# Optimization experiments

Hardware: AMD Instinct MI355X
Metric: run time of the kernel (lower is better)

## Reference

```python
import jax, jax.numpy as jnp
import numpy as np

VOCAB = 50000
D = 128      # word_embedding_size
H = 64       # attention_hidden_dim


def _doc_embed(words, emb_table, w_self, b_self):
    """words: (..., W) int -> (..., D) via tanh self-attention pooling over words."""
    we = emb_table[words]                                # (..., W, D)
    scores = jnp.tanh(we @ w_self + b_self)              # (..., W, 1)
    wgt = jax.nn.softmax(scores, axis=-2)                # softmax over word dim
    return jnp.sum(wgt * we, axis=-2)                    # (..., D)


def _attention(reviews_emb, query_emb, Wq, bq, w_red):
    """reviews_emb: (B,R,D), query_emb: (B,1,D) -> (B,D)."""
    B = query_emb.shape[0]
    pq = jnp.tanh(query_emb.reshape(B, D) @ Wq + bq)     # (B, D*H)
    pq = pq.reshape(B, D, H)
    s = jnp.einsum('brd,bdh->brh', reviews_emb, pq)      # (B,R,H)
    r = s @ w_red                                        # (B,R,1)
    w = jax.nn.softmax(r, axis=1)                        # softmax over reviews
    return jnp.sum(w * reviews_emb, axis=1)              # (B,D)


def setup_inputs() -> dict:
    key = jax.random.key(0)
    ks = jax.random.split(key, 9)
    B, R, W = 256, 20, 100
    user = jax.random.randint(ks[0], (B, R, W), 0, VOCAB)
    item = jax.random.randint(ks[1], (B, R, W), 0, VOCAB)
    query = jax.random.randint(ks[2], (B, W), 0, VOCAB)
    emb_table = jax.random.normal(ks[3], (VOCAB, D), dtype=jnp.float32) * 0.01
    w_self = jax.random.normal(ks[4], (D, 1), dtype=jnp.float32) * (1.0 / np.sqrt(D))
    b_self = jax.random.uniform(ks[5], (1,), dtype=jnp.float32, maxval=0.01)
    Wq = jax.random.normal(ks[6], (D, D * H), dtype=jnp.float32) * (1.0 / np.sqrt(D))
    bq = jax.random.uniform(ks[7], (D * H,), dtype=jnp.float32, maxval=0.01)
    w_red = jax.random.normal(ks[8], (H, 1), dtype=jnp.float32) * (1.0 / np.sqrt(H))
    pf = jnp.float32(0.5)  # personalized_factor
    return {"user_reviews_words": user, "item_reviews_words": item, "query": query,
            "emb_table": emb_table, "w_self": w_self, "b_self": b_self,
            "Wq": Wq, "bq": bq, "w_red": w_red, "pf": pf}


def reference(user_reviews_words, item_reviews_words, query,
              emb_table, w_self, b_self, Wq, bq, w_red, pf):
    # mode == 'test'
    user_emb = _doc_embed(user_reviews_words, emb_table, w_self, b_self)   # (B,R,D)
    item_emb = _doc_embed(item_reviews_words, emb_table, w_self, b_self)   # (B,R,D)
    q_emb = _doc_embed(query[:, None, :], emb_table, w_self, b_self)       # (B,1,D)
    user_entity = _attention(user_emb, q_emb, Wq, bq, w_red)               # (B,D)
    item_entity = _attention(item_emb, q_emb, Wq, bq, w_red)               # (B,D)
    personalized = user_entity + pf * q_emb[:, 0, :]
    return (personalized, item_entity)
```

## Files before the change

### kernel.cpp

```cpp
#include <hip/hip_runtime.h>
#include <math.h>

#define D 128
#define H 64
#define W 100
#define R 20
#define NB 256
#define NDOC_UI (NB * R)
#define VOCAB 50000

__device__ __forceinline__ float fast_tanh(float x) {
    float u = __expf(2.0f * x);
    return 1.0f - 2.0f * __builtin_amdgcn_rcpf(1.0f + u);
}
__device__ __forceinline__ float fast_exp_tanh(float x) {
    return __expf(fast_tanh(x));
}

__device__ __forceinline__ unsigned short f2bf(float f) {
    unsigned int b = __float_as_uint(f);
    b += 0x7fffu + ((b >> 16) & 1u);
    return (unsigned short)(b >> 16);
}

__global__ __launch_bounds__(256) void vocab_prep_kernel(
    const float* __restrict__ emb, const float* __restrict__ w_self,
    const float* __restrict__ b_self,
    ushort* __restrict__ emb_bf, float* __restrict__ evocab)
{
    int tid = threadIdx.x, lane32 = tid & 31, grp = tid >> 5;
    int row = blockIdx.x * 8 + grp;
    float4 v   = ((const float4*)emb)[row * 32 + lane32];
    float4 ws4 = ((const float4*)w_self)[lane32];
    float p = v.x * ws4.x + v.y * ws4.y + v.z * ws4.z + v.w * ws4.w;
    p += __shfl_xor(p, 16, 64);
    p += __shfl_xor(p, 8, 64);
    p += __shfl_xor(p, 4, 64);
    p += __shfl_xor(p, 2, 64);
    p += __shfl_xor(p, 1, 64);
    float e = __expf(tanhf(p + b_self[0]));
    if (lane32 == 0) evocab[row] = e;
    ushort4 u;
    u.x = f2bf(v.x * e); u.y = f2bf(v.y * e);
    u.z = f2bf(v.z * e); u.w = f2bf(v.w * e);
    ((ushort4*)emb_bf)[row * 32 + lane32] = u;
}

__global__ __launch_bounds__(128) void doc_embed_bf16_kernel(
    const int* __restrict__ user_w, const int* __restrict__ item_w,
    const int* __restrict__ query_w,
    const ushort* __restrict__ emb_bf, const float* __restrict__ evocab,
    float* __restrict__ user_emb, float* __restrict__ item_emb,
    float* __restrict__ q_emb)
{
    int tid    = threadIdx.x;
    int lane32 = tid & 31;
    int grp    = tid >> 5;
    int doc    = blockIdx.x * 4 + grp;

    const int* wp; float* outp;
    if (doc < NDOC_UI)        { wp = user_w + doc * W;               outp = user_emb + doc * D; }
    else if (doc < 2*NDOC_UI) { int t = doc - NDOC_UI;   wp = item_w  + t * W; outp = item_emb + t * D; }
    else                      { int t = doc - 2*NDOC_UI; wp = query_w + t * W; outp = q_emb    + t * D; }

    int wreg[4];
    #pragma unroll
    for (int k = 0; k < 4; ++k) {
        int idx = k * 32 + lane32;
        wreg[k] = wp[idx > W - 1 ? W - 1 : idx];
    }

    float ep = 0.f;
    #pragma unroll
    for (int k = 0; k < 4; ++k) {
        float e = evocab[wreg[k]];
        if (k < 3 || lane32 < 4) ep += e;
    }
    ep += __shfl_xor(ep, 16, 64);
    ep += __shfl_xor(ep, 8, 64);
    ep += __shfl_xor(ep, 4, 64);
    ep += __shfl_xor(ep, 2, 64);
    ep += __shfl_xor(ep, 1, 64);
    float inv = 1.f / ep;

    int permbase = (tid & 32) << 2;
    int sub      = lane32 >> 4;
    int quad     = lane32 & 15;

    float acc[8];
    #pragma unroll
    for (int j = 0; j < 8; ++j) acc[j] = 0.f;

    const uint4* ebf4 = (const uint4*)emb_bf;

    #pragma unroll
    for (int c = 0; c < 5; ++c) {
        int wid[10]; uint4 v[10];
        #pragma unroll
        for (int j = 0; j < 10; ++j) {
            int s = c * 10 + j;
            int lane_src = ((2 * s) & 31) | sub;
            wid[j] = __builtin_amdgcn_ds_bpermute(permbase | (lane_src << 2),
                                                  wreg[s >> 4]);
        }
        #pragma unroll
        for (int j = 0; j < 10; ++j)
            v[j] = ebf4[(size_t)(unsigned)wid[j] * 16 + quad];
        #pragma unroll
        for (int j = 0; j < 10; ++j) {
            uint4 x = v[j];
            acc[0] += __uint_as_float(x.x << 16);
            acc[1] += __uint_as_float(x.x & 0xffff0000u);
            acc[2] += __uint_as_float(x.y << 16);
            acc[3] += __uint_as_float(x.y & 0xffff0000u);
            acc[4] += __uint_as_float(x.z << 16);
            acc[5] += __uint_as_float(x.z & 0xffff0000u);
            acc[6] += __uint_as_float(x.w << 16);
            acc[7] += __uint_as_float(x.w & 0xffff0000u);
        }
    }

    #pragma unroll
    for (int j = 0; j < 8; ++j) acc[j] += __shfl_xor(acc[j], 16, 64);

    if (lane32 < 16) {
        float4 o0 = make_float4(acc[0]*inv, acc[1]*inv, acc[2]*inv, acc[3]*inv);
        float4 o1 = make_float4(acc[4]*inv, acc[5]*inv, acc[6]*inv, acc[7]*inv);
        ((float4*)outp)[quad * 2]     = o0;
        ((float4*)outp)[quad * 2 + 1] = o1;
    }
}

__global__ __launch_bounds__(256, 7) void doc_embed_fp32_kernel(
    const int* __restrict__ user_w, const int* __restrict__ item_w,
    const int* __restrict__ query_w,
    const float* __restrict__ emb, const float* __restrict__ w_self,
    const float* __restrict__ b_self,
    float* __restrict__ user_emb, float* __restrict__ item_emb,
    float* __restrict__ q_emb)
{
    int tid    = threadIdx.x;
    int lane32 = tid & 31;
    int grp    = tid >> 5;
    int doc    = blockIdx.x * 8 + grp;

    const int* wp; float* outp;
    if (doc < NDOC_UI)        { wp = user_w + doc * W;               outp = user_emb + doc * D; }
    else if (doc < 2*NDOC_UI) { int t = doc - NDOC_UI;   wp = item_w  + t * W; outp = item_emb + t * D; }
    else                      { int t = doc - 2*NDOC_UI; wp = query_w + t * W; outp = q_emb    + t * D; }

    int wreg[4];
    #pragma unroll
    for (int k = 0; k < 4; ++k) {
        int idx = k * 32 + lane32;
        wreg[k] = wp[idx > W - 1 ? W - 1 : idx];
    }

    float4 ws4 = ((const float4*)w_self)[lane32];
    float  bs  = b_self[0];
    const float4* emb4 = (const float4*)emb;
    int permbase = (tid & 32) * 4;

    float4 acc  = make_float4(0.f, 0.f, 0.f, 0.f);
    float  esum = 0.f;

    #pragma unroll
    for (int c = 0; c < 10; ++c) {
        int word[10];
        #pragma unroll
        for (int j = 0; j < 10; ++j) {
            int w = c * 10 + j;
            word[j] = __builtin_amdgcn_ds_bpermute(permbase | ((w & 31) * 4),
                                                   wreg[w >> 5]);
        }
        float4 v[10];
        #pragma unroll
        for (int j = 0; j < 10; ++j)
            v[j] = emb4[(size_t)word[j] * 32 + lane32];

        #pragma unroll
        for (int j = 0; j < 10; ++j) {
            float p = v[j].x * ws4.x + v[j].y * ws4.y + v[j].z * ws4.z + v[j].w * ws4.w;
            p += __shfl_xor(p, 16, 64);
            p += __shfl_xor(p, 8, 64);
            p += __shfl_xor(p, 4, 64);
            p += __shfl_xor(p, 2, 64);
            p += __shfl_xor(p, 1, 64);
            float e = fast_exp_tanh(p + bs);
            esum += e;
            acc.x += e * v[j].x;
            acc.y += e * v[j].y;
            acc.z += e * v[j].z;
            acc.w += e * v[j].w;
        }
    }

    float inv = 1.0f / esum;
    acc.x *= inv; acc.y *= inv; acc.z *= inv; acc.w *= inv;
    ((float4*)outp)[lane32] = acc;
}

__global__ __launch_bounds__(256) void pv_kernel(
    const float* __restrict__ q_emb, const float* __restrict__ Wq,
    const float* __restrict__ bq, const float* __restrict__ w_red,
    float* __restrict__ pv)
{
    __shared__ __align__(16) float Wb[128 * 68];

    int dd  = blockIdx.x;
    int m0g = blockIdx.y * 128;
    int tid = threadIdx.x;

    {
        int rrow = tid >> 4;
        int f4   = tid & 15;
        #pragma unroll
        for (int pass = 0; pass < 8; ++pass) {
            int k = pass * 16 + rrow;
            float4 vw = ((const float4*)Wq)[k * 2048 + dd * 16 + f4];
            *(float4*)&Wb[k * 68 + f4 * 4] = vw;
        }
    }
    __syncthreads();

    int nthr = tid & 15;
    int mthr = tid >> 4;
    int n0 = nthr * 4;
    const float4* q4 = (const float4*)q_emb;
    int mbase = (m0g + mthr * 8) * 32;

    float acc[8][4];
    #pragma unroll
    for (int i = 0; i < 8; ++i)
        #pragma unroll
        for (int j = 0; j < 4; ++j) acc[i][j] = 0.f;

    float4 qa[8], qb[8];
    #pragma unroll
    for (int i = 0; i < 8; ++i) qa[i] = q4[mbase + i * 32];

    for (int k4 = 0; k4 < 32; ++k4) {
        if (k4 < 31) {
            #pragma unroll
            for (int i = 0; i < 8; ++i) qb[i] = q4[mbase + i * 32 + k4 + 1];
        }
        #pragma unroll
        for (int kk = 0; kk < 4; ++kk) {
            float4 wv = *(const float4*)&Wb[(k4 * 4 + kk) * 68 + n0];
            #pragma unroll
            for (int i = 0; i < 8; ++i) {
                float a = (kk == 0) ? qa[i].x : (kk == 1) ? qa[i].y
                        : (kk == 2) ? qa[i].z : qa[i].w;
                acc[i][0] += a * wv.x;
                acc[i][1] += a * wv.y;
                acc[i][2] += a * wv.z;
                acc[i][3] += a * wv.w;
            }
        }
        #pragma unroll
        for (int i = 0; i < 8; ++i) qa[i] = qb[i];
    }

    float4 bqv = ((const float4*)bq)[dd * 16 + nthr];
    float4 wrv = ((const float4*)w_red)[nthr];

    #pragma unroll
    for (int i = 0; i < 8; ++i) {
        float s = fast_tanh(acc[i][0] + bqv.x) * wrv.x
                + fast_tanh(acc[i][1] + bqv.y) * wrv.y
                + fast_tanh(acc[i][2] + bqv.z) * wrv.z
                + fast_tanh(acc[i][3] + bqv.w) * wrv.w;
        s += __shfl_xor(s, 1, 64);
        s += __shfl_xor(s, 2, 64);
        s += __shfl_xor(s, 4, 64);
        s += __shfl_xor(s, 8, 64);
        if (nthr == 0) pv[(m0g + mthr * 8 + i) * 128 + dd] = s;
    }
}

__global__ __launch_bounds__(256) void attn_kernel(
    const float* __restrict__ user_emb, const float* __restrict__ item_emb,
    const float* __restrict__ q_emb, const float* __restrict__ pv,
    const float* __restrict__ pf, float* __restrict__ out)
{
    __shared__ float rev[R * 129];
    __shared__ float pvl[D];
    __shared__ float sc[R];

    int b   = blockIdx.x;
    int set = blockIdx.y;
    const float* revg = (set == 0 ? user_emb : item_emb) + b * R * D;
    int tid = threadIdx.x;

    for (int idx = tid; idx < R * D; idx += 256)
        rev[(idx >> 7) * 129 + (idx & 127)] = revg[idx];
    if (tid < D) pvl[tid] = pv[b * D + tid];
    __syncthreads();

    if (tid < R) {
        float s = 0.f;
        const float* row = &rev[tid * 129];
        #pragma unroll 16
        for (int k = 0; k < D; ++k) s += row[k] * pvl[k];
        sc[tid] = s;
    }
    __syncthreads();

    float m = -1e30f;
    for (int r = 0; r < R; ++r) m = fmaxf(m, sc[r]);
    float sum = 0.f;
    for (int r = 0; r < R; ++r) sum += __expf(sc[r] - m);
    float inv = 1.f / sum;

    if (tid < D) {
        float acc = 0.f;
        for (int r = 0; r < R; ++r)
            acc += __expf(sc[r] - m) * inv * rev[r * 129 + tid];
        if (set == 0) {
            acc += pf[0] * q_emb[b * D + tid];
            out[b * D + tid] = acc;
        } else {
            out[NB * D + b * D + tid] = acc;
        }
    }
}

extern "C" void kernel_launch(void* const* d_in, const int* in_sizes, int n_in,
                              void* d_out, int out_size, void* d_ws, size_t ws_size,
                              hipStream_t stream) {
    const int*   user_w  = (const int*)d_in[0];
    const int*   item_w  = (const int*)d_in[1];
    const int*   query_w = (const int*)d_in[2];
    const float* emb     = (const float*)d_in[3];
    const float* w_self  = (const float*)d_in[4];
    const float* b_self  = (const float*)d_in[5];
    const float* Wq      = (const float*)d_in[6];
    const float* bq      = (const float*)d_in[7];
    const float* w_red   = (const float*)d_in[8];
    const float* pf      = (const float*)d_in[9];

    float* ws       = (float*)d_ws;
    float* user_emb = ws;
    float* item_emb = user_emb + NDOC_UI * D;
    float* q_emb    = item_emb + NDOC_UI * D;
    float* pv       = q_emb    + NB * D;
    float* evocab   = pv       + NB * D;
    ushort* emb_bf  = (ushort*)(evocab + VOCAB);
    float* out      = (float*)d_out;

    const size_t need_fast =
        (size_t)(2 * NDOC_UI * D + 2 * NB * D + VOCAB) * sizeof(float)
        + (size_t)VOCAB * D * sizeof(ushort);

    if (ws_size >= need_fast) {
        vocab_prep_kernel<<<VOCAB / 8, 256, 0, stream>>>(
            emb, w_self, b_self, emb_bf, evocab);
        doc_embed_bf16_kernel<<<(2 * NDOC_UI + NB) / 4, 128, 0, stream>>>(
            user_w, item_w, query_w, emb_bf, evocab, user_emb, item_emb, q_emb);
    } else {
        doc_embed_fp32_kernel<<<(2 * NDOC_UI + NB) / 8, 256, 0, stream>>>(
            user_w, item_w, query_w, emb, w_self, b_self, user_emb, item_emb, q_emb);
    }
    pv_kernel<<<dim3(128, 2), 256, 0, stream>>>(q_emb, Wq, bq, w_red, pv);
    attn_kernel<<<dim3(NB, 2), 256, 0, stream>>>(user_emb, item_emb, q_emb, pv, pf, out);
}
```

Baseline: 152.7 us.

## Split bf16 embedding table into column halves pinned to XCD groups for L2 locality

The prescaled bf16 embedding table is now stored as two column halves of 64 features each. The doc-embed grid is doubled, and block indices are mapped so that four XCDs process one half and the other four process the other half. Each XCD's L2 then only has to cache about half of the gathered table (around 6.4MB instead of 12.8MB), which should raise hit rates on the random gathers. The cost is that every word index and every evocab normalisation sum is now read and computed twice, and each 32-lane group covers 4 words × 8 lanes with an extra shuffle-reduce step.

```diff
diff --git a/kernel.cpp b/kernel.cpp
--- a/kernel.cpp
+++ b/kernel.cpp
@@ -7,6 +7,7 @@
 #define R 20
 #define NB 256
 #define NDOC_UI (NB * R)
+#define NDOC    (2 * NDOC_UI + NB)
 #define VOCAB 50000
 
 __device__ __forceinline__ float fast_tanh(float x) {
@@ -43,7 +44,9 @@
     ushort4 u;
     u.x = f2bf(v.x * e); u.y = f2bf(v.y * e);
     u.z = f2bf(v.z * e); u.w = f2bf(v.w * e);
-    ((ushort4*)emb_bf)[row * 32 + lane32] = u;
+    int half = lane32 >> 4;
+    ushort4* dst = (ushort4*)(emb_bf + (size_t)half * VOCAB * 64);
+    dst[row * 16 + (lane32 & 15)] = u;
 }
 
 __global__ __launch_bounds__(128) void doc_embed_bf16_kernel(
@@ -56,7 +59,11 @@
     int tid    = threadIdx.x;
     int lane32 = tid & 31;
     int grp    = tid >> 5;
-    int doc    = blockIdx.x * 4 + grp;
+    unsigned B   = blockIdx.x;
+    unsigned xcd = B & 7;
+    unsigned half= xcd >> 2;
+    unsigned sub = (B >> 3) * 4 + (xcd & 3);
+    int doc = (int)sub * 4 + grp;
 
     const int* wp; float* outp;
     if (doc < NDOC_UI)        { wp = user_w + doc * W;               outp = user_emb + doc * D; }
@@ -84,30 +91,28 @@
     float inv = 1.f / ep;
 
     int permbase = (tid & 32) << 2;
-    int sub      = lane32 >> 4;
-    int quad     = lane32 & 15;
+    int wsub     = lane32 >> 3;
+    int oct      = lane32 & 7;
 
     float acc[8];
     #pragma unroll
     for (int j = 0; j < 8; ++j) acc[j] = 0.f;
 
-    const uint4* ebf4 = (const uint4*)emb_bf;
-
-    #pragma unroll
-    for (int c = 0; c < 5; ++c) {
-        int wid[10]; uint4 v[10];
-        #pragma unroll
-        for (int j = 0; j < 10; ++j) {
-            int s = c * 10 + j;
-            int lane_src = ((2 * s) & 31) | sub;
-            wid[j] = __builtin_amdgcn_ds_bpermute(permbase | (lane_src << 2),
-                                                  wreg[s >> 4]);
-        }
-        #pragma unroll
-        for (int j = 0; j < 10; ++j)
-            v[j] = ebf4[(size_t)(unsigned)wid[j] * 16 + quad];
-        #pragma unroll
-        for (int j = 0; j < 10; ++j) {
+    const uint4* eb4 = (const uint4*)(emb_bf + (size_t)half * VOCAB * 64);
+
+    #pragma unroll
+    for (int c = 0; c < 2; ++c) {
+        const int n = (c == 0) ? 13 : 12;
+        const int s0 = (c == 0) ? 0 : 13;
+        int wid[13]; uint4 v[13];
+        for (int j = 0; j < n; ++j) {
+            int s = s0 + j;
+            wid[j] = __builtin_amdgcn_ds_bpermute(
+                permbase | ((((4 * s) & 31) + wsub) << 2), wreg[s >> 3]);
+        }
+        for (int j = 0; j < n; ++j)
+            v[j] = eb4[(size_t)(unsigned)wid[j] * 8 + oct];
+        for (int j = 0; j < n; ++j) {
             uint4 x = v[j];
             acc[0] += __uint_as_float(x.x << 16);
             acc[1] += __uint_as_float(x.x & 0xffff0000u);
@@ -121,13 +126,15 @@
     }
 
     #pragma unroll
-    for (int j = 0; j < 8; ++j) acc[j] += __shfl_xor(acc[j], 16, 64);
-
-    if (lane32 < 16) {
-        float4 o0 = make_float4(acc[0]*inv, acc[1]*inv, acc[2]*inv, acc[3]*inv);
-        float4 o1 = make_float4(acc[4]*inv, acc[5]*inv, acc[6]*inv, acc[7]*inv);
-        ((float4*)outp)[quad * 2]     = o0;
-        ((float4*)outp)[quad * 2 + 1] = o1;
+    for (int j = 0; j < 8; ++j) {
+        acc[j] += __shfl_xor(acc[j], 8, 64);
+        acc[j] += __shfl_xor(acc[j], 16, 64);
+    }
+
+    if (wsub == 0) {
+        float* o = outp + half * 64 + oct * 8;
+        *(float4*)o       = make_float4(acc[0]*inv, acc[1]*inv, acc[2]*inv, acc[3]*inv);
+        *(float4*)(o + 4) = make_float4(acc[4]*inv, acc[5]*inv, acc[6]*inv, acc[7]*inv);
     }
 }
 
@@ -355,10 +362,10 @@
     if (ws_size >= need_fast) {
         vocab_prep_kernel<<<VOCAB / 8, 256, 0, stream>>>(
             emb, w_self, b_self, emb_bf, evocab);
-        doc_embed_bf16_kernel<<<(2 * NDOC_UI + NB) / 4, 128, 0, stream>>>(
+        doc_embed_bf16_kernel<<<NDOC * 2 / 4, 128, 0, stream>>>(
             user_w, item_w, query_w, emb_bf, evocab, user_emb, item_emb, q_emb);
     } else {
-        doc_embed_fp32_kernel<<<(2 * NDOC_UI + NB) / 8, 256, 0, stream>>>(
+        doc_embed_fp32_kernel<<<NDOC / 8, 256, 0, stream>>>(
             user_w, item_w, query_w, emb, w_self, b_self, user_emb, item_emb, q_emb);
     }
     pv_kernel<<<dim3(128, 2), 256, 0, stream>>>(q_emb, Wq, bq, w_red, pv);
```

New measurement: 149.0 us. 1.02x faster.
